# Kernel optimization log

Hardware: AMD Instinct MI355X
Metric: run time of the kernel (lower is better)

Reference implementation:

```python
import jax, jax.numpy as jnp
import numpy as np

B, NQ, NA, C, L = 8, 2048, 64, 128, 4  # batches, queries/mol, atoms/mol, hidden, num_layers
CUTOFF = 8.0
E_AQ, E_QQ = 131072, 262144


def _ln(x, g, b):
    m = x.mean(-1, keepdims=True)
    v = ((x - m) ** 2).mean(-1, keepdims=True)
    return (x - m) * jax.lax.rsqrt(v + 1e-5) * g + b


def _egnn(p, h_src, h_tgt, pos_src, pos_tgt, t_emb, esrc, etgt):
    (mW1, mb1, mW2, mb2, cW1, cb1, cW2, cb2, nW1, nb1, nW2, nb2, g, b) = p
    rel = pos_tgt[etgt] - pos_src[esrc]                      # (E,3)
    sq = (rel ** 2).sum(-1, keepdims=True)                   # (E,1)
    mi = jnp.concatenate([h_src[esrc], h_tgt[etgt], sq, t_emb[etgt]], -1)  # (E,3C+1)
    msg = jax.nn.silu(jax.nn.silu(mi @ mW1 + mb1) @ mW2 + mb2)             # (E,C)
    w = jnp.tanh(jax.nn.silu(msg @ cW1 + cb1) @ cW2 + cb2)                 # (E,1)
    vel = jnp.zeros_like(pos_tgt).at[etgt].add(w * rel)
    agg = jnp.zeros_like(h_tgt).at[etgt].add(msg)
    u = jnp.concatenate([h_tgt, agg], -1)
    h_new = _ln(h_tgt + (jax.nn.silu(u @ nW1 + nb1) @ nW2 + nb2), g, b)
    return h_new, vel


def setup_inputs() -> dict:
    key = jax.random.key(0)
    ks = iter(jax.random.split(key, 64))
    n = lambda shape, s=0.05: jax.random.normal(next(ks), shape, dtype=jnp.float32) * s
    NQT, NAT = B * NQ, B * NA
    return dict(
        x_t=jax.random.normal(next(ks), (NQT, 3), dtype=jnp.float32) * 3.0,
        t_query=jax.random.uniform(next(ks), (NQT,), dtype=jnp.float32),
        atom_pos=jax.random.normal(next(ks), (NAT, 3), dtype=jnp.float32) * 3.0,
        atom_feat=n((NAT, 256), 1.0),
        edge_aq_src=jax.random.randint(next(ks), (E_AQ,), 0, NAT, dtype=jnp.int32),
        edge_aq_tgt=jax.random.randint(next(ks), (E_AQ,), 0, NQT, dtype=jnp.int32),
        edge_qq_src=jax.random.randint(next(ks), (E_QQ,), 0, NQT, dtype=jnp.int32),
        edge_qq_tgt=jax.random.randint(next(ks), (E_QQ,), 0, NQT, dtype=jnp.int32),
        atom_proj_W=n((256, C)), atom_proj_b=jnp.zeros((C,)),
        time_W1=n((C, 4 * C)), time_b1=jnp.zeros((4 * C,)),
        time_W2=n((4 * C, C)), time_b2=jnp.zeros((C,)),
        qi_W1=n((1, C)), qi_b1=jnp.zeros((C,)),
        qi_W2=n((C, C)), qi_b2=jnp.zeros((C,)),
        msg_W1=n((2 * L, 3 * C + 1, 2 * C)), msg_b1=jnp.zeros((2 * L, 2 * C)),
        msg_W2=n((2 * L, 2 * C, C)), msg_b2=jnp.zeros((2 * L, C)),
        cw_W1=n((2 * L, C, C // 2)), cw_b1=jnp.zeros((2 * L, C // 2)),
        cw_W2=n((2 * L, C // 2, 1)), cw_b2=jnp.zeros((2 * L, 1)),
        nu_W1=n((2 * L, 2 * C, C)), nu_b1=jnp.zeros((2 * L, C)),
        nu_W2=n((2 * L, C, C)), nu_b2=jnp.zeros((2 * L, C)),
        ln_g=jnp.ones((2 * L, C)), ln_b=jnp.zeros((2 * L, C)),
        vo_W1=n((C, C)), vo_b1=jnp.zeros((C,)),
        vo_W2=n((C, 1)), vo_b2=jnp.zeros((1,)),
    )


def reference(x_t, t_query, atom_pos, atom_feat,
              edge_aq_src, edge_aq_tgt, edge_qq_src, edge_qq_tgt,
              atom_proj_W, atom_proj_b,
              time_W1, time_b1, time_W2, time_b2,
              qi_W1, qi_b1, qi_W2, qi_b2,
              msg_W1, msg_b1, msg_W2, msg_b2,
              cw_W1, cw_b1, cw_W2, cw_b2,
              nu_W1, nu_b1, nu_W2, nu_b2,
              ln_g, ln_b,
              vo_W1, vo_b1, vo_W2, vo_b2):
    # atom features (no condition drop: eval mode)
    h_atom = atom_feat @ atom_proj_W + atom_proj_b

    # sinusoidal time embedding per query node
    half = C // 2
    freqs = jnp.exp(-np.log(10000.0) * jnp.arange(half, dtype=jnp.float32) / (half - 1))
    args = t_query[:, None] * freqs[None, :]
    emb = jnp.concatenate([jnp.sin(args), jnp.cos(args)], -1)
    t_emb = jax.nn.silu(emb @ time_W1 + time_b1) @ time_W2 + time_b2

    # init query features: log1p(mean_dist / cutoff), equal-size batches
    q = x_t.reshape(B, NQ, 3)
    a = atom_pos.reshape(B, NA, 3)
    sq = ((q[:, :, None, :] - a[:, None, :, :]) ** 2).sum(-1)  # (B,NQ,NA)
    log_dist = jnp.log1p(jnp.sqrt(sq.mean(-1)) / CUTOFF).reshape(-1, 1)
    h = jax.nn.silu(log_dist @ qi_W1 + qi_b1) @ qi_W2 + qi_b2

    layers = (msg_W1, msg_b1, msg_W2, msg_b2, cw_W1, cw_b1, cw_W2, cw_b2,
              nu_W1, nu_b1, nu_W2, nu_b2, ln_g, ln_b)
    pick = lambda j: tuple(arr[j] for arr in layers)

    vel = jnp.zeros_like(x_t)
    for i in range(L):
        h, dv = _egnn(pick(2 * i), h_atom, h, atom_pos, x_t, t_emb, edge_aq_src, edge_aq_tgt)
        vel = vel + dv
        h, dv = _egnn(pick(2 * i + 1), h, h, x_t, x_t, t_emb, edge_qq_src, edge_qq_tgt)
        vel = vel + dv

    scale = jax.nn.silu(h @ vo_W1 + vo_b1) @ vo_W2 + vo_b2   # (N_q,1)
    return vel * scale
```

## Files before the change

kernel.cpp:

```cpp
#include <hip/hip_runtime.h>

#define NQT 16384
#define NAT 512
#define EAQ 131072
#define EQQ 262144

typedef short short8 __attribute__((ext_vector_type(8)));
typedef float float4v __attribute__((ext_vector_type(4)));

__device__ __forceinline__ float silu_f(float x){ return x / (1.f + __expf(-x)); }

__device__ __forceinline__ short f2bf(float f){
  union { float f; unsigned u; } v; v.f = f;
  unsigned r = v.u + 0x7fff + ((v.u >> 16) & 1);
  return (short)(r >> 16);
}
__device__ __forceinline__ float bf2f(short s){
  union { unsigned u; float f; } v;
  v.u = ((unsigned)(unsigned short)s) << 16;
  return v.f;
}

__global__ __launch_bounds__(256) void k_hist(
    const int* __restrict__ etgt, int* __restrict__ hist, int E)
{
  int i = blockIdx.x*256 + threadIdx.x;
  if (i < E) atomicAdd(&hist[etgt[i]], 1);
}

__global__ __launch_bounds__(256) void k_scan(int* __restrict__ hist)
{
  __shared__ int part[256];
  int t = threadIdx.x;
  int base = t * 64;
  int s = 0;
  for (int i = 0; i < 64; i++) s += hist[base + i];
  part[t] = s;
  __syncthreads();
  for (int off = 1; off < 256; off <<= 1){
    int v = (t >= off) ? part[t - off] : 0;
    __syncthreads();
    part[t] += v;
    __syncthreads();
  }
  int run = (t == 0) ? 0 : part[t-1];
  for (int i = 0; i < 64; i++){
    int h = hist[base + i];
    hist[base + i] = run;
    run += h;
  }
}

__global__ __launch_bounds__(256) void k_place(
    const int* __restrict__ esrc, const int* __restrict__ etgt,
    int* __restrict__ cursor, int2* __restrict__ desc, int E)
{
  int i = blockIdx.x*256 + threadIdx.x;
  if (i < E){
    int tg = etgt[i];
    int pos = atomicAdd(&cursor[tg], 1);
    desc[pos] = make_int2(esrc[i], tg);
  }
}

__global__ __launch_bounds__(256) void k_pack(
    const float* __restrict__ W, short* __restrict__ out,
    int rows, int cols, int ksteps, int ntiles, int total, int mode)
{
  int idx = blockIdx.x * 256 + threadIdx.x;
  if (idx >= total) return;
  int l8   = idx & 7;
  int lane = (idx >> 3) & 63;
  int kk   = (idx >> 9) % ksteps;
  int nt   = ((idx >> 9) / ksteps) % ntiles;
  int j    = idx / (512 * ksteps * ntiles);
  int k = kk*32 + (lane >> 4)*8 + l8;
  if (mode == 1) k += (k >= 256);
  else if (mode == 2) k = (k < 128) ? k + 128 : k + 129;
  int n = nt*16 + (lane & 15);
  out[idx] = f2bf(W[(size_t)j*rows*cols + (size_t)k*cols + n]);
}

template<int KSTEPS>
__global__ __launch_bounds__(256) void k_pre(
    const float* __restrict__ Xa, const float* __restrict__ Xb,
    const float* __restrict__ bias,
    const short* __restrict__ Wp, short* __restrict__ out)
{
  int t = threadIdx.x;
  int lane = t & 63, w = t >> 6;
  int mrow = lane & 15, quad = lane >> 4;
  int m0 = blockIdx.x*64 + w*16;

  short8 areg[KSTEPS];
  #pragma unroll
  for (int kk = 0; kk < KSTEPS; kk++){
    int k = kk*32 + quad*8;
    const float* bp;
    if (KSTEPS == 8 && kk >= 4) bp = Xb + (size_t)(m0+mrow)*128 + (k - 128);
    else                        bp = Xa + (size_t)(m0+mrow)*128 + k;
    float4 f0 = *(const float4*)(bp);
    float4 f1 = *(const float4*)(bp + 4);
    short8 s;
    s[0]=f2bf(f0.x); s[1]=f2bf(f0.y); s[2]=f2bf(f0.z); s[3]=f2bf(f0.w);
    s[4]=f2bf(f1.x); s[5]=f2bf(f1.y); s[6]=f2bf(f1.z); s[7]=f2bf(f1.w);
    areg[kk] = s;
  }
  #pragma unroll
  for (int nt = 0; nt < 16; nt++){
    float4v acc = {0.f,0.f,0.f,0.f};
    const short8* Bb = (const short8*)(Wp + ((size_t)nt*KSTEPS)*512 + lane*8);
    #pragma unroll
    for (int kk = 0; kk < KSTEPS; kk++)
      acc = __builtin_amdgcn_mfma_f32_16x16x32_bf16(areg[kk], Bb[kk*64], acc, 0, 0, 0);
    float bv = bias ? bias[nt*16 + mrow] : 0.f;
    #pragma unroll
    for (int r = 0; r < 4; r++)
      out[(size_t)(m0 + quad*4 + r)*256 + nt*16 + mrow] = f2bf(acc[r] + bv);
  }
}

__global__ __launch_bounds__(128) void k_hatom(
    const float* __restrict__ feat, const float* __restrict__ W,
    const float* __restrict__ b, float* __restrict__ out)
{
  __shared__ float sf[256];
  int n = blockIdx.x, t = threadIdx.x;
  sf[t]       = feat[n*256 + t];
  sf[t + 128] = feat[n*256 + 128 + t];
  __syncthreads();
  float acc = b[t];
  for (int k = 0; k < 256; k++) acc += sf[k] * W[k*128 + t];
  out[n*128 + t] = acc;
}

__global__ __launch_bounds__(256) void k_temb(
    const float* __restrict__ tq,
    const short* __restrict__ W1p, const float* __restrict__ b1,
    const short* __restrict__ W2p, const float* __restrict__ b2,
    float* __restrict__ temb)
{
  __shared__ __align__(16) short A[32*136];
  __shared__ __align__(16) short B[32*528];
  int t = threadIdx.x;
  int n0 = blockIdx.x * 32;

  {
    int row = t >> 3, l = t & 7;
    float tv = tq[n0 + row];
    short* o = A + row*136;
    #pragma unroll
    for (int i = 0; i < 16; i++){
      int k = l*16 + i;
      int h = k & 63;
      float freq = __expf(-9.210340371976184f * (float)h * (1.f/63.f));
      float a = tv * freq;
      float v = (k < 64) ? __sinf(a) : __cosf(a);
      o[k] = f2bf(v);
    }
  }
  __syncthreads();

  int lane = t & 63, w = t >> 6;
  int mrow = lane & 15, quad = lane >> 4;

  for (int nti = 0; nti < 8; nti++){
    int nt = w*8 + nti;
    #pragma unroll
    for (int mt = 0; mt < 2; mt++){
      float4v acc = {0.f,0.f,0.f,0.f};
      const short8* Ab = (const short8*)(A + (mt*16 + mrow)*136 + quad*8);
      const short8* Bb = (const short8*)(W1p + (size_t)nt*4*512 + lane*8);
      #pragma unroll
      for (int kk = 0; kk < 4; kk++)
        acc = __builtin_amdgcn_mfma_f32_16x16x32_bf16(Ab[kk*4], Bb[kk*64], acc, 0, 0, 0);
      int n = nt*16 + mrow;
      float b1n = b1[n];
      #pragma unroll
      for (int r = 0; r < 4; r++)
        B[(mt*16 + quad*4 + r)*528 + n] = f2bf(silu_f(acc[r] + b1n));
    }
  }
  __syncthreads();

  #pragma unroll
  for (int nti = 0; nti < 2; nti++){
    int nt = w*2 + nti;
    #pragma unroll
    for (int mt = 0; mt < 2; mt++){
      float4v acc = {0.f,0.f,0.f,0.f};
      const short8* Ab = (const short8*)(B + (mt*16 + mrow)*528 + quad*8);
      const short8* Bb = (const short8*)(W2p + (size_t)nt*16*512 + lane*8);
      #pragma unroll
      for (int kk = 0; kk < 16; kk++)
        acc = __builtin_amdgcn_mfma_f32_16x16x32_bf16(Ab[kk*4], Bb[kk*64], acc, 0, 0, 0);
      int n = nt*16 + mrow;
      float b2n = b2[n];
      #pragma unroll
      for (int r = 0; r < 4; r++)
        temb[(size_t)(n0 + mt*16 + quad*4 + r)*128 + n] = acc[r] + b2n;
    }
  }
}

__global__ __launch_bounds__(128) void k_hinit(
    const float* __restrict__ x_t, const float* __restrict__ atom_pos,
    const float* __restrict__ W1, const float* __restrict__ b1,
    const float* __restrict__ W2, const float* __restrict__ b2,
    float* __restrict__ h)
{
  __shared__ float sh[128];
  __shared__ float sld;
  int n = blockIdx.x, t = threadIdx.x;
  float qx = x_t[n*3], qy = x_t[n*3+1], qz = x_t[n*3+2];
  float part = 0.f;
  if (t < 64){
    int a = (n >> 11)*64 + t;
    float dx = qx - atom_pos[a*3];
    float dy = qy - atom_pos[a*3+1];
    float dz = qz - atom_pos[a*3+2];
    part = dx*dx + dy*dy + dz*dz;
  }
  #pragma unroll
  for (int off = 32; off; off >>= 1) part += __shfl_down(part, off);
  if (t == 0) sld = log1pf(sqrtf(part * (1.f/64.f)) * 0.125f);
  __syncthreads();
  float ld = sld;
  sh[t] = silu_f(ld * W1[t] + b1[t]);
  __syncthreads();
  float acc = b2[t];
  for (int k = 0; k < 128; k++) acc += sh[k] * W2[k*128 + t];
  h[(size_t)n*128 + t] = acc;
}

__global__ __launch_bounds__(256) void k_edge(
    const short* __restrict__ Psrc, const short* __restrict__ Ptgt,
    const float* __restrict__ pos_src, const float* __restrict__ pos_tgt,
    const int2* __restrict__ sdesc,
    const float* __restrict__ w1sq,
    const short* __restrict__ W2p, const float* __restrict__ b2,
    const short* __restrict__ W3p, const float* __restrict__ b3,
    const float* __restrict__ W4,  const float* __restrict__ b4,
    float* __restrict__ agg, float* __restrict__ vel)
{
  __shared__ __align__(16) short A2[32*264];
  __shared__ __align__(16) short A3[32*136];
  __shared__ float sw1[256];
  __shared__ float rel_s[32*3];
  __shared__ int   tgt_s[32];
  float* h3 = (float*)A2;

  int t = threadIdx.x;
  int e0 = blockIdx.x * 32;

  sw1[t] = w1sq[t];
  __syncthreads();

  {
    int e = t >> 3, l = t & 7;
    int2 d = sdesc[e0 + e];
    int src = d.x, tgt = d.y;
    float rx = pos_tgt[tgt*3+0] - pos_src[src*3+0];
    float ry = pos_tgt[tgt*3+1] - pos_src[src*3+1];
    float rz = pos_tgt[tgt*3+2] - pos_src[src*3+2];
    float sqv = rx*rx + ry*ry + rz*rz;
    if (l == 0){
      rel_s[e*3+0]=rx; rel_s[e*3+1]=ry; rel_s[e*3+2]=rz;
      tgt_s[e] = tgt;
    }
    const short8* ps = (const short8*)(Psrc + (size_t)src*256);
    const short8* pt = (const short8*)(Ptgt + (size_t)tgt*256);
    #pragma unroll
    for (int c = 0; c < 4; c++){
      int ci = c*8 + l;
      int n0 = ci*8;
      short8 a = ps[ci], b = pt[ci];
      short8 r;
      #pragma unroll
      for (int j = 0; j < 8; j++){
        int n = n0 + j;
        float v = bf2f(a[j]) + bf2f(b[j]) + sqv*sw1[n];
        r[j] = f2bf(silu_f(v));
      }
      *(short8*)(A2 + e*264 + n0) = r;
    }
  }
  __syncthreads();

  int lane = t & 63, w = t >> 6;
  int mrow = lane & 15, quad = lane >> 4;

  float4v acc2[2][2];
  #pragma unroll
  for (int nti = 0; nti < 2; nti++){
    int nt = w*2 + nti;
    #pragma unroll
    for (int mt = 0; mt < 2; mt++){
      float4v acc = {0.f,0.f,0.f,0.f};
      const short8* Ab = (const short8*)(A2 + (mt*16 + mrow)*264 + quad*8);
      const short8* Bb = (const short8*)(W2p + (size_t)nt*8*512 + lane*8);
      #pragma unroll
      for (int kk = 0; kk < 8; kk++)
        acc = __builtin_amdgcn_mfma_f32_16x16x32_bf16(Ab[kk*4], Bb[kk*64], acc, 0, 0, 0);
      acc2[nti][mt] = acc;
    }
  }

  #pragma unroll
  for (int nti = 0; nti < 2; nti++){
    int nt = w*2 + nti;
    int n = nt*16 + mrow;
    float b2n = b2[n];
    #pragma unroll
    for (int mt = 0; mt < 2; mt++){
      #pragma unroll
      for (int r = 0; r < 4; r++){
        int e = mt*16 + quad*4 + r;
        A3[e*136 + n] = f2bf(silu_f(acc2[nti][mt][r] + b2n));
      }
    }
  }
  __syncthreads();

  {
    int c = t & 127, hh = t >> 7;
    int eb = hh*16;
    float run = 0.f;
    int cur = tgt_s[eb];
    for (int e = eb; e < eb + 16; e++){
      int tg = tgt_s[e];
      if (tg != cur){
        atomicAdd(&agg[(size_t)cur*128 + c], run);
        run = 0.f; cur = tg;
      }
      run += bf2f(A3[e*136 + c]);
    }
    atomicAdd(&agg[(size_t)cur*128 + c], run);
  }
  __syncthreads();

  {
    int nt = w;
    #pragma unroll
    for (int mt = 0; mt < 2; mt++){
      float4v acc = {0.f,0.f,0.f,0.f};
      const short8* Ab = (const short8*)(A3 + (mt*16 + mrow)*136 + quad*8);
      const short8* Bb = (const short8*)(W3p + (size_t)nt*4*512 + lane*8);
      #pragma unroll
      for (int kk = 0; kk < 4; kk++)
        acc = __builtin_amdgcn_mfma_f32_16x16x32_bf16(Ab[kk*4], Bb[kk*64], acc, 0, 0, 0);
      int n = nt*16 + mrow;
      float b3n = b3[n];
      #pragma unroll
      for (int r = 0; r < 4; r++){
        int e = mt*16 + quad*4 + r;
        h3[e*68 + n] = silu_f(acc[r] + b3n);
      }
    }
  }
  __syncthreads();

  {
    int e = t >> 3, l = t & 7;
    float p = 0.f;
    #pragma unroll
    for (int i = 0; i < 8; i++){
      int k = l + 8*i;
      p += h3[e*68 + k] * W4[k];
    }
    p += __shfl_xor(p, 1);
    p += __shfl_xor(p, 2);
    p += __shfl_xor(p, 4);
    if (l == 0){
      float wv = tanhf(p + b4[0]);
      int tg = tgt_s[e];
      atomicAdd(&vel[tg*3+0], wv*rel_s[e*3+0]);
      atomicAdd(&vel[tg*3+1], wv*rel_s[e*3+1]);
      atomicAdd(&vel[tg*3+2], wv*rel_s[e*3+2]);
    }
  }
}

__global__ __launch_bounds__(256) void k_node(
    const float* __restrict__ h, const float* __restrict__ agg,
    const short* __restrict__ W1p, const float* __restrict__ b1,
    const short* __restrict__ W2p, const float* __restrict__ b2,
    const float* __restrict__ g, const float* __restrict__ bb_,
    float* __restrict__ h_out)
{
  __shared__ __align__(16) short A[32*264];
  __shared__ __align__(16) short B[32*136];
  float* r = (float*)A;
  int t = threadIdx.x;
  int n0 = blockIdx.x * 32;

  {
    int row = t >> 3, l = t & 7;
    const float4* hr = (const float4*)(h   + (size_t)(n0+row)*128);
    const float4* ar = (const float4*)(agg + (size_t)(n0+row)*128);
    short* o = A + row*264;
    #pragma unroll
    for (int i = 0; i < 4; i++){
      int k4 = l + 8*i;
      float4 a = hr[k4], b = ar[k4];
      short8 s;
      s[0]=f2bf(a.x); s[1]=f2bf(a.y); s[2]=f2bf(a.z); s[3]=f2bf(a.w);
      s[4]=f2bf(b.x); s[5]=f2bf(b.y); s[6]=f2bf(b.z); s[7]=f2bf(b.w);
      *(short8*)(o + k4*4)       = (short8){s[0],s[1],s[2],s[3],0,0,0,0};
    }
  }
  {
    int row = t >> 3, l = t & 7;
    const float4* hr = (const float4*)(h   + (size_t)(n0+row)*128);
    const float4* ar = (const float4*)(agg + (size_t)(n0+row)*128);
    short* o = A + row*264;
    #pragma unroll
    for (int i = 0; i < 4; i++){
      int k4 = l + 8*i;
      float4 a = hr[k4];
      short4 s4;
      short sa0=f2bf(a.x), sa1=f2bf(a.y), sa2=f2bf(a.z), sa3=f2bf(a.w);
      o[k4*4+0]=sa0; o[k4*4+1]=sa1; o[k4*4+2]=sa2; o[k4*4+3]=sa3;
      float4 b = ar[k4];
      o[128 + k4*4+0]=f2bf(b.x); o[128 + k4*4+1]=f2bf(b.y);
      o[128 + k4*4+2]=f2bf(b.z); o[128 + k4*4+3]=f2bf(b.w);
    }
  }
  __syncthreads();

  int lane = t & 63, w = t >> 6;
  int mrow = lane & 15, quad = lane >> 4;

  float4v accA[2][2];
  #pragma unroll
  for (int nti = 0; nti < 2; nti++){
    int nt = w*2 + nti;
    #pragma unroll
    for (int mt = 0; mt < 2; mt++){
      float4v acc = {0.f,0.f,0.f,0.f};
      const short8* Ab = (const short8*)(A + (mt*16 + mrow)*264 + quad*8);
      const short8* Bb = (const short8*)(W1p + (size_t)nt*8*512 + lane*8);
      #pragma unroll
      for (int kk = 0; kk < 8; kk++)
        acc = __builtin_amdgcn_mfma_f32_16x16x32_bf16(Ab[kk*4], Bb[kk*64], acc, 0, 0, 0);
      accA[nti][mt] = acc;
    }
  }
  __syncthreads();

  #pragma unroll
  for (int nti = 0; nti < 2; nti++){
    int n = (w*2 + nti)*16 + mrow;
    float b1n = b1[n];
    #pragma unroll
    for (int mt = 0; mt < 2; mt++){
      #pragma unroll
      for (int rr = 0; rr < 4; rr++){
        int e = mt*16 + quad*4 + rr;
        B[e*136 + n] = f2bf(silu_f(accA[nti][mt][rr] + b1n));
      }
    }
  }
  __syncthreads();

  #pragma unroll
  for (int nti = 0; nti < 2; nti++){
    int nt = w*2 + nti;
    #pragma unroll
    for (int mt = 0; mt < 2; mt++){
      float4v acc = {0.f,0.f,0.f,0.f};
      const short8* Ab = (const short8*)(B + (mt*16 + mrow)*136 + quad*8);
      const short8* Bb = (const short8*)(W2p + (size_t)nt*4*512 + lane*8);
      #pragma unroll
      for (int kk = 0; kk < 4; kk++)
        acc = __builtin_amdgcn_mfma_f32_16x16x32_bf16(Ab[kk*4], Bb[kk*64], acc, 0, 0, 0);
      int n = nt*16 + mrow;
      float b2n = b2[n];
      #pragma unroll
      for (int rr = 0; rr < 4; rr++){
        int e = mt*16 + quad*4 + rr;
        r[e*132 + n] = h[(size_t)(n0+e)*128 + n] + acc[rr] + b2n;
      }
    }
  }
  __syncthreads();

  {
    int lane2 = t & 63, wid = t >> 6;
    #pragma unroll
    for (int nn = 0; nn < 8; nn++){
      int row = wid*8 + nn;
      float a = r[row*132 + lane2], bv = r[row*132 + lane2 + 64];
      float s = a + bv, ss = a*a + bv*bv;
      #pragma unroll
      for (int off = 1; off < 64; off <<= 1){
        s  += __shfl_xor(s, off);
        ss += __shfl_xor(ss, off);
      }
      float mean = s * (1.f/128.f);
      float var  = ss * (1.f/128.f) - mean*mean;
      float rstd = rsqrtf(var + 1e-5f);
      float* ho = h_out + (size_t)(n0+row)*128;
      ho[lane2]      = (a  - mean)*rstd*g[lane2]      + bb_[lane2];
      ho[lane2 + 64] = (bv - mean)*rstd*g[lane2 + 64] + bb_[lane2 + 64];
    }
  }
}

__global__ __launch_bounds__(128) void k_out(
    const float* __restrict__ h, const float* __restrict__ vel,
    const float* __restrict__ W1, const float* __restrict__ b1,
    const float* __restrict__ W2, const float* __restrict__ b2,
    float* __restrict__ out)
{
  __shared__ float sh[128];
  __shared__ float spart[2];
  int n = blockIdx.x, t = threadIdx.x;
  sh[t] = h[(size_t)n*128 + t];
  __syncthreads();
  float acc = b1[t];
  for (int k = 0; k < 128; k++) acc += sh[k] * W1[k*128 + t];
  float p = silu_f(acc) * W2[t];
  #pragma unroll
  for (int off = 32; off; off >>= 1) p += __shfl_down(p, off);
  if ((t & 63) == 0) spart[t >> 6] = p;
  __syncthreads();
  if (t < 3){
    float scale = spart[0] + spart[1] + b2[0];
    out[n*3 + t] = vel[n*3 + t] * scale;
  }
}

extern "C" void kernel_launch(void* const* d_in, const int* in_sizes, int n_in,
                              void* d_out, int out_size, void* d_ws, size_t ws_size,
                              hipStream_t stream)
{
  const float* x_t       = (const float*)d_in[0];
  const float* t_query   = (const float*)d_in[1];
  const float* atom_pos  = (const float*)d_in[2];
  const float* atom_feat = (const float*)d_in[3];
  const int*   e_aq_s = (const int*)d_in[4];
  const int*   e_aq_t = (const int*)d_in[5];
  const int*   e_qq_s = (const int*)d_in[6];
  const int*   e_qq_t = (const int*)d_in[7];
  const float* apW  = (const float*)d_in[8];
  const float* apb  = (const float*)d_in[9];
  const float* tW1  = (const float*)d_in[10];
  const float* tb1  = (const float*)d_in[11];
  const float* tW2  = (const float*)d_in[12];
  const float* tb2  = (const float*)d_in[13];
  const float* qiW1 = (const float*)d_in[14];
  const float* qib1 = (const float*)d_in[15];
  const float* qiW2 = (const float*)d_in[16];
  const float* qib2 = (const float*)d_in[17];
  const float* mW1  = (const float*)d_in[18];
  const float* mb1  = (const float*)d_in[19];
  const float* mW2  = (const float*)d_in[20];
  const float* mb2  = (const float*)d_in[21];
  const float* cW1  = (const float*)d_in[22];
  const float* cb1  = (const float*)d_in[23];
  const float* cW2  = (const float*)d_in[24];
  const float* cb2  = (const float*)d_in[25];
  const float* nW1  = (const float*)d_in[26];
  const float* nb1  = (const float*)d_in[27];
  const float* nW2  = (const float*)d_in[28];
  const float* nb2  = (const float*)d_in[29];
  const float* lng  = (const float*)d_in[30];
  const float* lnb  = (const float*)d_in[31];
  const float* voW1 = (const float*)d_in[32];
  const float* vob1 = (const float*)d_in[33];
  const float* voW2 = (const float*)d_in[34];
  const float* vob2 = (const float*)d_in[35];
  float* out = (float*)d_out;

  float* ws     = (float*)d_ws;
  float* h_atom = ws;
  float* temb   = h_atom + 65536;
  float* hA     = temb + 2097152;
  float* hB     = hA + 2097152;
  float* agg    = hB + 2097152;
  float* vel    = agg + 2097152;
  short* W1ap   = (short*)(vel + 49152);
  short* W1bcp  = W1ap + 262144;
  short* W2p    = W1bcp + 524288;
  short* W3p    = W2p + 262144;
  short* nW1p   = W3p + 65536;
  short* nW2p   = nW1p + 262144;
  short* tW1p   = nW2p + 131072;
  short* tW2p   = tW1p + 65536;
  short* Psrc   = tW2p + 65536;
  short* Ptgt   = Psrc + 4194304;
  int*   hist_a = (int*)(Ptgt + 4194304);
  int*   hist_q = hist_a + 16384;
  int2*  desc_a = (int2*)(hist_q + 16384);
  int2*  desc_q = desc_a + EAQ;

  hipMemsetAsync(hist_a, 0, 16384*sizeof(int), stream);
  hipMemsetAsync(hist_q, 0, 16384*sizeof(int), stream);
  k_hist<<<EAQ/256, 256, 0, stream>>>(e_aq_t, hist_a, EAQ);
  k_hist<<<EQQ/256, 256, 0, stream>>>(e_qq_t, hist_q, EQQ);
  k_scan<<<1, 256, 0, stream>>>(hist_a);
  k_scan<<<1, 256, 0, stream>>>(hist_q);
  k_place<<<EAQ/256, 256, 0, stream>>>(e_aq_s, e_aq_t, hist_a, desc_a, EAQ);
  k_place<<<EQQ/256, 256, 0, stream>>>(e_qq_s, e_qq_t, hist_q, desc_q, EQQ);

  k_pack<<<(262144+255)/256, 256, 0, stream>>>(mW1, W1ap,  385, 256, 4, 16, 262144, 0);
  k_pack<<<(524288+255)/256, 256, 0, stream>>>(mW1, W1bcp, 385, 256, 8, 16, 524288, 2);
  k_pack<<<(262144+255)/256, 256, 0, stream>>>(mW2, W2p,   256, 128, 8,  8, 262144, 0);
  k_pack<<<( 65536+255)/256, 256, 0, stream>>>(cW1, W3p,   128,  64, 4,  4,  65536, 0);
  k_pack<<<(262144+255)/256, 256, 0, stream>>>(nW1, nW1p,  256, 128, 8,  8, 262144, 0);
  k_pack<<<(131072+255)/256, 256, 0, stream>>>(nW2, nW2p,  128, 128, 4,  8, 131072, 0);
  k_pack<<<( 65536+255)/256, 256, 0, stream>>>(tW1, tW1p,  128, 512, 4, 32,  65536, 0);
  k_pack<<<( 65536+255)/256, 256, 0, stream>>>(tW2, tW2p,  512, 128, 16, 8,  65536, 0);

  hipMemsetAsync(vel, 0, (size_t)NQT*3*sizeof(float), stream);
  k_hatom<<<NAT, 128, 0, stream>>>(atom_feat, apW, apb, h_atom);
  k_temb<<<NQT/32, 256, 0, stream>>>(t_query, tW1p, tb1, tW2p, tb2, temb);
  k_hinit<<<NQT, 128, 0, stream>>>(x_t, atom_pos, qiW1, qib1, qiW2, qib2, hA);

  float* hc = hA; float* hn = hB;
  for (int i = 0; i < 4; i++){
    for (int half = 0; half < 2; half++){
      int j = 2*i + half;
      const int2* dsc = half ? desc_q : desc_a;
      int E = half ? EQQ : EAQ;
      const float* hsrc = half ? hc : h_atom;
      int Msrc = half ? NQT : NAT;

      k_pre<4><<<Msrc/64, 256, 0, stream>>>(hsrc, nullptr, nullptr,
          W1ap + (size_t)j*32768, Psrc);
      k_pre<8><<<NQT/64, 256, 0, stream>>>(hc, temb, mb1 + (size_t)j*256,
          W1bcp + (size_t)j*65536, Ptgt);

      hipMemsetAsync(agg, 0, (size_t)NQT*128*sizeof(float), stream);
      k_edge<<<E/32, 256, 0, stream>>>(Psrc, Ptgt,
          half ? x_t : atom_pos, x_t, dsc,
          mW1 + (size_t)j*385*256 + 65536,
          W2p + (size_t)j*32768, mb2 + (size_t)j*128,
          W3p + (size_t)j*8192,  cb1 + (size_t)j*64,
          cW2 + (size_t)j*64,    cb2 + (size_t)j,
          agg, vel);
      k_node<<<NQT/32, 256, 0, stream>>>(hc, agg,
          nW1p + (size_t)j*32768, nb1 + (size_t)j*128,
          nW2p + (size_t)j*16384, nb2 + (size_t)j*128,
          lng + (size_t)j*128,    lnb + (size_t)j*128, hn);
      float* tmp = hc; hc = hn; hn = tmp;
    }
  }
  k_out<<<NQT, 128, 0, stream>>>(hc, vel, voW1, vob1, voW2, vob2, out);
}
```

Before: 1.433 ms.

## Merge setup launches, fuse pre-GEMMs, widen edge kernel, zero agg in node kernel

Merges the histogram, scan, place and weight-pack launches into single kernels, and fuses the two per-layer projection GEMMs into one launch to cut launch overhead. The edge kernel moves to 512 threads with one n-tile per wave and reads the squared-distance weight directly from global memory instead of staging it in shared memory. Messages are aggregated from an fp32 copy rather than bf16, and the coordinate-MLP MFMA is issued before the scatter. The node kernel now zeroes agg after reading it, which removes the per-layer memset, so correctness depends on the first memset also covering agg and vel.

```diff
diff --git a/kernel.cpp b/kernel.cpp
--- a/kernel.cpp
+++ b/kernel.cpp
@@ -21,15 +21,18 @@
   return v.f;
 }
 
-__global__ __launch_bounds__(256) void k_hist(
-    const int* __restrict__ etgt, int* __restrict__ hist, int E)
+__global__ __launch_bounds__(256) void k_hist2(
+    const int* __restrict__ ta, const int* __restrict__ tq,
+    int* __restrict__ ha, int* __restrict__ hq)
 {
   int i = blockIdx.x*256 + threadIdx.x;
-  if (i < E) atomicAdd(&hist[etgt[i]], 1);
-}
-
-__global__ __launch_bounds__(256) void k_scan(int* __restrict__ hist)
-{
+  atomicAdd(&hq[tq[i]], 1);
+  if (i < EAQ) atomicAdd(&ha[ta[i]], 1);
+}
+
+__global__ __launch_bounds__(256) void k_scan2(int* __restrict__ ha, int* __restrict__ hq)
+{
+  int* hist = (blockIdx.x == 0) ? ha : hq;
   __shared__ int part[256];
   int t = threadIdx.x;
   int base = t * 64;
@@ -51,24 +54,21 @@
   }
 }
 
-__global__ __launch_bounds__(256) void k_place(
-    const int* __restrict__ esrc, const int* __restrict__ etgt,
-    int* __restrict__ cursor, int2* __restrict__ desc, int E)
+__global__ __launch_bounds__(256) void k_place2(
+    const int* __restrict__ sa, const int* __restrict__ ta,
+    const int* __restrict__ sq, const int* __restrict__ tq,
+    int* __restrict__ ca, int* __restrict__ cq,
+    int2* __restrict__ da, int2* __restrict__ dq)
 {
   int i = blockIdx.x*256 + threadIdx.x;
-  if (i < E){
-    int tg = etgt[i];
-    int pos = atomicAdd(&cursor[tg], 1);
-    desc[pos] = make_int2(esrc[i], tg);
-  }
-}
-
-__global__ __launch_bounds__(256) void k_pack(
+  { int tg = tq[i]; int pos = atomicAdd(&cq[tg], 1); dq[pos] = make_int2(sq[i], tg); }
+  if (i < EAQ){ int tg = ta[i]; int pos = atomicAdd(&ca[tg], 1); da[pos] = make_int2(sa[i], tg); }
+}
+
+__device__ __forceinline__ void pack_one(
     const float* __restrict__ W, short* __restrict__ out,
-    int rows, int cols, int ksteps, int ntiles, int total, int mode)
-{
-  int idx = blockIdx.x * 256 + threadIdx.x;
-  if (idx >= total) return;
+    int rows, int cols, int ksteps, int ntiles, int idx, int mode)
+{
   int l8   = idx & 7;
   int lane = (idx >> 3) & 63;
   int kk   = (idx >> 9) % ksteps;
@@ -81,42 +81,86 @@
   out[idx] = f2bf(W[(size_t)j*rows*cols + (size_t)k*cols + n]);
 }
 
-template<int KSTEPS>
-__global__ __launch_bounds__(256) void k_pre(
-    const float* __restrict__ Xa, const float* __restrict__ Xb,
-    const float* __restrict__ bias,
-    const short* __restrict__ Wp, short* __restrict__ out)
+__global__ __launch_bounds__(256) void k_packall(
+    const float* __restrict__ mW1, const float* __restrict__ mW2,
+    const float* __restrict__ cW1, const float* __restrict__ nW1,
+    const float* __restrict__ nW2, const float* __restrict__ tW1,
+    const float* __restrict__ tW2,
+    short* W1ap, short* W1bcp, short* W2p, short* W3p,
+    short* nW1p, short* nW2p, short* tW1p, short* tW2p)
+{
+  int b = blockIdx.x, t = threadIdx.x;
+  if (b < 1024){ pack_one(mW1, W1ap, 385,256,4,16, b*256+t, 0); return; } b -= 1024;
+  if (b < 2048){ pack_one(mW1, W1bcp,385,256,8,16, b*256+t, 2); return; } b -= 2048;
+  if (b < 1024){ pack_one(mW2, W2p,  256,128,8, 8, b*256+t, 0); return; } b -= 1024;
+  if (b <  256){ pack_one(cW1, W3p,  128, 64,4, 4, b*256+t, 0); return; } b -=  256;
+  if (b < 1024){ pack_one(nW1, nW1p, 256,128,8, 8, b*256+t, 0); return; } b -= 1024;
+  if (b <  512){ pack_one(nW2, nW2p, 128,128,4, 8, b*256+t, 0); return; } b -=  512;
+  if (b <  256){ pack_one(tW1, tW1p, 128,512,4,32, b*256+t, 0); return; } b -=  256;
+  pack_one(tW2, tW2p, 512,128,16,8, b*256+t, 0);
+}
+
+__global__ __launch_bounds__(256) void k_pre2(
+    const float* __restrict__ Xsrc, const float* __restrict__ Xh,
+    const float* __restrict__ Xt, const float* __restrict__ biasT,
+    const short* __restrict__ WpA, const short* __restrict__ WpB,
+    short* __restrict__ Psrc, short* __restrict__ Ptgt, int nblkA)
 {
   int t = threadIdx.x;
   int lane = t & 63, w = t >> 6;
   int mrow = lane & 15, quad = lane >> 4;
-  int m0 = blockIdx.x*64 + w*16;
-
-  short8 areg[KSTEPS];
-  #pragma unroll
-  for (int kk = 0; kk < KSTEPS; kk++){
-    int k = kk*32 + quad*8;
-    const float* bp;
-    if (KSTEPS == 8 && kk >= 4) bp = Xb + (size_t)(m0+mrow)*128 + (k - 128);
-    else                        bp = Xa + (size_t)(m0+mrow)*128 + k;
-    float4 f0 = *(const float4*)(bp);
-    float4 f1 = *(const float4*)(bp + 4);
-    short8 s;
-    s[0]=f2bf(f0.x); s[1]=f2bf(f0.y); s[2]=f2bf(f0.z); s[3]=f2bf(f0.w);
-    s[4]=f2bf(f1.x); s[5]=f2bf(f1.y); s[6]=f2bf(f1.z); s[7]=f2bf(f1.w);
-    areg[kk] = s;
-  }
-  #pragma unroll
-  for (int nt = 0; nt < 16; nt++){
-    float4v acc = {0.f,0.f,0.f,0.f};
-    const short8* Bb = (const short8*)(Wp + ((size_t)nt*KSTEPS)*512 + lane*8);
-    #pragma unroll
-    for (int kk = 0; kk < KSTEPS; kk++)
-      acc = __builtin_amdgcn_mfma_f32_16x16x32_bf16(areg[kk], Bb[kk*64], acc, 0, 0, 0);
-    float bv = bias ? bias[nt*16 + mrow] : 0.f;
-    #pragma unroll
-    for (int r = 0; r < 4; r++)
-      out[(size_t)(m0 + quad*4 + r)*256 + nt*16 + mrow] = f2bf(acc[r] + bv);
+
+  if ((int)blockIdx.x < nblkA){
+    int m0 = blockIdx.x*64 + w*16;
+    short8 areg[4];
+    #pragma unroll
+    for (int kk = 0; kk < 4; kk++){
+      const float* bp = Xsrc + (size_t)(m0+mrow)*128 + kk*32 + quad*8;
+      float4 f0 = *(const float4*)(bp);
+      float4 f1 = *(const float4*)(bp + 4);
+      short8 s;
+      s[0]=f2bf(f0.x); s[1]=f2bf(f0.y); s[2]=f2bf(f0.z); s[3]=f2bf(f0.w);
+      s[4]=f2bf(f1.x); s[5]=f2bf(f1.y); s[6]=f2bf(f1.z); s[7]=f2bf(f1.w);
+      areg[kk] = s;
+    }
+    #pragma unroll
+    for (int nt = 0; nt < 16; nt++){
+      float4v acc = {0.f,0.f,0.f,0.f};
+      const short8* Bb = (const short8*)(WpA + ((size_t)nt*4)*512 + lane*8);
+      #pragma unroll
+      for (int kk = 0; kk < 4; kk++)
+        acc = __builtin_amdgcn_mfma_f32_16x16x32_bf16(areg[kk], Bb[kk*64], acc, 0, 0, 0);
+      #pragma unroll
+      for (int r = 0; r < 4; r++)
+        Psrc[(size_t)(m0 + quad*4 + r)*256 + nt*16 + mrow] = f2bf(acc[r]);
+    }
+  } else {
+    int m0 = ((int)blockIdx.x - nblkA)*64 + w*16;
+    short8 areg[8];
+    #pragma unroll
+    for (int kk = 0; kk < 8; kk++){
+      int k = kk*32 + quad*8;
+      const float* bp = (kk >= 4) ? (Xt + (size_t)(m0+mrow)*128 + (k - 128))
+                                  : (Xh + (size_t)(m0+mrow)*128 + k);
+      float4 f0 = *(const float4*)(bp);
+      float4 f1 = *(const float4*)(bp + 4);
+      short8 s;
+      s[0]=f2bf(f0.x); s[1]=f2bf(f0.y); s[2]=f2bf(f0.z); s[3]=f2bf(f0.w);
+      s[4]=f2bf(f1.x); s[5]=f2bf(f1.y); s[6]=f2bf(f1.z); s[7]=f2bf(f1.w);
+      areg[kk] = s;
+    }
+    #pragma unroll
+    for (int nt = 0; nt < 16; nt++){
+      float4v acc = {0.f,0.f,0.f,0.f};
+      const short8* Bb = (const short8*)(WpB + ((size_t)nt*8)*512 + lane*8);
+      #pragma unroll
+      for (int kk = 0; kk < 8; kk++)
+        acc = __builtin_amdgcn_mfma_f32_16x16x32_bf16(areg[kk], Bb[kk*64], acc, 0, 0, 0);
+      float bv = biasT[nt*16 + mrow];
+      #pragma unroll
+      for (int r = 0; r < 4; r++)
+        Ptgt[(size_t)(m0 + quad*4 + r)*256 + nt*16 + mrow] = f2bf(acc[r] + bv);
+    }
   }
 }
 
@@ -233,7 +277,7 @@
   h[(size_t)n*128 + t] = acc;
 }
 
-__global__ __launch_bounds__(256) void k_edge(
+__global__ __launch_bounds__(512, 8) void k_edge(
     const short* __restrict__ Psrc, const short* __restrict__ Ptgt,
     const float* __restrict__ pos_src, const float* __restrict__ pos_tgt,
     const int2* __restrict__ sdesc,
@@ -245,19 +289,16 @@
 {
   __shared__ __align__(16) short A2[32*264];
   __shared__ __align__(16) short A3[32*136];
-  __shared__ float sw1[256];
   __shared__ float rel_s[32*3];
   __shared__ int   tgt_s[32];
-  float* h3 = (float*)A2;
+  float* msgf = (float*)A2;
+  float* h3   = (float*)A2;
 
   int t = threadIdx.x;
   int e0 = blockIdx.x * 32;
 
-  sw1[t] = w1sq[t];
-  __syncthreads();
-
-  {
-    int e = t >> 3, l = t & 7;
+  {
+    int e = t >> 4, l = t & 15;
     int2 d = sdesc[e0 + e];
     int src = d.x, tgt = d.y;
     float rx = pos_tgt[tgt*3+0] - pos_src[src*3+0];
@@ -271,17 +312,21 @@
     const short8* ps = (const short8*)(Psrc + (size_t)src*256);
     const short8* pt = (const short8*)(Ptgt + (size_t)tgt*256);
     #pragma unroll
-    for (int c = 0; c < 4; c++){
-      int ci = c*8 + l;
+    for (int c = 0; c < 2; c++){
+      int ci = l + 16*c;
       int n0 = ci*8;
       short8 a = ps[ci], b = pt[ci];
+      float4 w0 = *(const float4*)(w1sq + n0);
+      float4 w1 = *(const float4*)(w1sq + n0 + 4);
       short8 r;
-      #pragma unroll
-      for (int j = 0; j < 8; j++){
-        int n = n0 + j;
-        float v = bf2f(a[j]) + bf2f(b[j]) + sqv*sw1[n];
-        r[j] = f2bf(silu_f(v));
-      }
+      r[0] = f2bf(silu_f(bf2f(a[0]) + bf2f(b[0]) + sqv*w0.x));
+      r[1] = f2bf(silu_f(bf2f(a[1]) + bf2f(b[1]) + sqv*w0.y));
+      r[2] = f2bf(silu_f(bf2f(a[2]) + bf2f(b[2]) + sqv*w0.z));
+      r[3] = f2bf(silu_f(bf2f(a[3]) + bf2f(b[3]) + sqv*w0.w));
+      r[4] = f2bf(silu_f(bf2f(a[4]) + bf2f(b[4]) + sqv*w1.x));
+      r[5] = f2bf(silu_f(bf2f(a[5]) + bf2f(b[5]) + sqv*w1.y));
+      r[6] = f2bf(silu_f(bf2f(a[6]) + bf2f(b[6]) + sqv*w1.z));
+      r[7] = f2bf(silu_f(bf2f(a[7]) + bf2f(b[7]) + sqv*w1.w));
       *(short8*)(A2 + e*264 + n0) = r;
     }
   }
@@ -290,10 +335,9 @@
   int lane = t & 63, w = t >> 6;
   int mrow = lane & 15, quad = lane >> 4;
 
-  float4v acc2[2][2];
-  #pragma unroll
-  for (int nti = 0; nti < 2; nti++){
-    int nt = w*2 + nti;
+  float4v acc2[2];
+  {
+    int nt = w;
     #pragma unroll
     for (int mt = 0; mt < 2; mt++){
       float4v acc = {0.f,0.f,0.f,0.f};
@@ -302,75 +346,78 @@
       #pragma unroll
       for (int kk = 0; kk < 8; kk++)
         acc = __builtin_amdgcn_mfma_f32_16x16x32_bf16(Ab[kk*4], Bb[kk*64], acc, 0, 0, 0);
-      acc2[nti][mt] = acc;
-    }
-  }
-
-  #pragma unroll
-  for (int nti = 0; nti < 2; nti++){
-    int nt = w*2 + nti;
-    int n = nt*16 + mrow;
+      acc2[mt] = acc;
+    }
+  }
+  __syncthreads();
+
+  {
+    int n = w*16 + mrow;
     float b2n = b2[n];
     #pragma unroll
     for (int mt = 0; mt < 2; mt++){
       #pragma unroll
       for (int r = 0; r < 4; r++){
         int e = mt*16 + quad*4 + r;
-        A3[e*136 + n] = f2bf(silu_f(acc2[nti][mt][r] + b2n));
+        float v = silu_f(acc2[mt][r] + b2n);
+        msgf[e*132 + n] = v;
+        A3[e*136 + n]   = f2bf(v);
       }
     }
   }
   __syncthreads();
 
-  {
-    int c = t & 127, hh = t >> 7;
-    int eb = hh*16;
+  int nt3 = w & 3, mt3 = w >> 2;
+  float4v acc3 = {0.f,0.f,0.f,0.f};
+  {
+    const short8* Ab = (const short8*)(A3 + (mt3*16 + mrow)*136 + quad*8);
+    const short8* Bb = (const short8*)(W3p + (size_t)nt3*4*512 + lane*8);
+    #pragma unroll
+    for (int kk = 0; kk < 4; kk++)
+      acc3 = __builtin_amdgcn_mfma_f32_16x16x32_bf16(Ab[kk*4], Bb[kk*64], acc3, 0, 0, 0);
+  }
+
+  {
+    int c = t & 127, g = t >> 7;
+    int eb = g*8;
     float run = 0.f;
     int cur = tgt_s[eb];
-    for (int e = eb; e < eb + 16; e++){
+    #pragma unroll
+    for (int e = eb; e < eb + 8; e++){
       int tg = tgt_s[e];
       if (tg != cur){
         atomicAdd(&agg[(size_t)cur*128 + c], run);
         run = 0.f; cur = tg;
       }
-      run += bf2f(A3[e*136 + c]);
+      run += msgf[e*132 + c];
     }
     atomicAdd(&agg[(size_t)cur*128 + c], run);
   }
   __syncthreads();
 
   {
-    int nt = w;
-    #pragma unroll
-    for (int mt = 0; mt < 2; mt++){
-      float4v acc = {0.f,0.f,0.f,0.f};
-      const short8* Ab = (const short8*)(A3 + (mt*16 + mrow)*136 + quad*8);
-      const short8* Bb = (const short8*)(W3p + (size_t)nt*4*512 + lane*8);
-      #pragma unroll
-      for (int kk = 0; kk < 4; kk++)
-        acc = __builtin_amdgcn_mfma_f32_16x16x32_bf16(Ab[kk*4], Bb[kk*64], acc, 0, 0, 0);
-      int n = nt*16 + mrow;
-      float b3n = b3[n];
-      #pragma unroll
-      for (int r = 0; r < 4; r++){
-        int e = mt*16 + quad*4 + r;
-        h3[e*68 + n] = silu_f(acc[r] + b3n);
-      }
-    }
-  }
-  __syncthreads();
-
-  {
-    int e = t >> 3, l = t & 7;
+    int n = nt3*16 + mrow;
+    float b3n = b3[n];
+    #pragma unroll
+    for (int r = 0; r < 4; r++){
+      int e = mt3*16 + quad*4 + r;
+      h3[e*68 + n] = silu_f(acc3[r] + b3n);
+    }
+  }
+  __syncthreads();
+
+  {
+    int e = t >> 4, l = t & 15;
     float p = 0.f;
     #pragma unroll
-    for (int i = 0; i < 8; i++){
-      int k = l + 8*i;
+    for (int i = 0; i < 4; i++){
+      int k = l + 16*i;
       p += h3[e*68 + k] * W4[k];
     }
     p += __shfl_xor(p, 1);
     p += __shfl_xor(p, 2);
     p += __shfl_xor(p, 4);
+    p += __shfl_xor(p, 8);
     if (l == 0){
       float wv = tanhf(p + b4[0]);
       int tg = tgt_s[e];
@@ -382,7 +429,7 @@
 }
 
 __global__ __launch_bounds__(256) void k_node(
-    const float* __restrict__ h, const float* __restrict__ agg,
+    const float* __restrict__ h, float* __restrict__ agg,
     const short* __restrict__ W1p, const float* __restrict__ b1,
     const short* __restrict__ W2p, const float* __restrict__ b2,
     const float* __restrict__ g, const float* __restrict__ bb_,
@@ -396,34 +443,19 @@
 
   {
     int row = t >> 3, l = t & 7;
-    const float4* hr = (const float4*)(h   + (size_t)(n0+row)*128);
-    const float4* ar = (const float4*)(agg + (size_t)(n0+row)*128);
+    const float4* hr = (const float4*)(h + (size_t)(n0+row)*128);
+    float4*       ar = (float4*)(agg + (size_t)(n0+row)*128);
     short* o = A + row*264;
-    #pragma unroll
-    for (int i = 0; i < 4; i++){
-      int k4 = l + 8*i;
-      float4 a = hr[k4], b = ar[k4];
-      short8 s;
-      s[0]=f2bf(a.x); s[1]=f2bf(a.y); s[2]=f2bf(a.z); s[3]=f2bf(a.w);
-      s[4]=f2bf(b.x); s[5]=f2bf(b.y); s[6]=f2bf(b.z); s[7]=f2bf(b.w);
-      *(short8*)(o + k4*4)       = (short8){s[0],s[1],s[2],s[3],0,0,0,0};
-    }
-  }
-  {
-    int row = t >> 3, l = t & 7;
-    const float4* hr = (const float4*)(h   + (size_t)(n0+row)*128);
-    const float4* ar = (const float4*)(agg + (size_t)(n0+row)*128);
-    short* o = A + row*264;
+    float4 z = make_float4(0.f,0.f,0.f,0.f);
     #pragma unroll
     for (int i = 0; i < 4; i++){
       int k4 = l + 8*i;
       float4 a = hr[k4];
-      short4 s4;
-      short sa0=f2bf(a.x), sa1=f2bf(a.y), sa2=f2bf(a.z), sa3=f2bf(a.w);
-      o[k4*4+0]=sa0; o[k4*4+1]=sa1; o[k4*4+2]=sa2; o[k4*4+3]=sa3;
+      o[k4*4+0]=f2bf(a.x); o[k4*4+1]=f2bf(a.y); o[k4*4+2]=f2bf(a.z); o[k4*4+3]=f2bf(a.w);
       float4 b = ar[k4];
       o[128 + k4*4+0]=f2bf(b.x); o[128 + k4*4+1]=f2bf(b.y);
       o[128 + k4*4+2]=f2bf(b.z); o[128 + k4*4+3]=f2bf(b.w);
+      ar[k4] = z;
     }
   }
   __syncthreads();
@@ -595,25 +627,16 @@
   int2*  desc_a = (int2*)(hist_q + 16384);
   int2*  desc_q = desc_a + EAQ;
 
-  hipMemsetAsync(hist_a, 0, 16384*sizeof(int), stream);
-  hipMemsetAsync(hist_q, 0, 16384*sizeof(int), stream);
-  k_hist<<<EAQ/256, 256, 0, stream>>>(e_aq_t, hist_a, EAQ);
-  k_hist<<<EQQ/256, 256, 0, stream>>>(e_qq_t, hist_q, EQQ);
-  k_scan<<<1, 256, 0, stream>>>(hist_a);
-  k_scan<<<1, 256, 0, stream>>>(hist_q);
-  k_place<<<EAQ/256, 256, 0, stream>>>(e_aq_s, e_aq_t, hist_a, desc_a, EAQ);
-  k_place<<<EQQ/256, 256, 0, stream>>>(e_qq_s, e_qq_t, hist_q, desc_q, EQQ);
-
-  k_pack<<<(262144+255)/256, 256, 0, stream>>>(mW1, W1ap,  385, 256, 4, 16, 262144, 0);
-  k_pack<<<(524288+255)/256, 256, 0, stream>>>(mW1, W1bcp, 385, 256, 8, 16, 524288, 2);
-  k_pack<<<(262144+255)/256, 256, 0, stream>>>(mW2, W2p,   256, 128, 8,  8, 262144, 0);
-  k_pack<<<( 65536+255)/256, 256, 0, stream>>>(cW1, W3p,   128,  64, 4,  4,  65536, 0);
-  k_pack<<<(262144+255)/256, 256, 0, stream>>>(nW1, nW1p,  256, 128, 8,  8, 262144, 0);
-  k_pack<<<(131072+255)/256, 256, 0, stream>>>(nW2, nW2p,  128, 128, 4,  8, 131072, 0);
-  k_pack<<<( 65536+255)/256, 256, 0, stream>>>(tW1, tW1p,  128, 512, 4, 32,  65536, 0);
-  k_pack<<<( 65536+255)/256, 256, 0, stream>>>(tW2, tW2p,  512, 128, 16, 8,  65536, 0);
-
-  hipMemsetAsync(vel, 0, (size_t)NQT*3*sizeof(float), stream);
+  hipMemsetAsync(hist_a, 0, 2*16384*sizeof(int), stream);
+  k_hist2<<<EQQ/256, 256, 0, stream>>>(e_aq_t, e_qq_t, hist_a, hist_q);
+  k_scan2<<<2, 256, 0, stream>>>(hist_a, hist_q);
+  k_place2<<<EQQ/256, 256, 0, stream>>>(e_aq_s, e_aq_t, e_qq_s, e_qq_t,
+                                        hist_a, hist_q, desc_a, desc_q);
+
+  k_packall<<<6400, 256, 0, stream>>>(mW1, mW2, cW1, nW1, nW2, tW1, tW2,
+      W1ap, W1bcp, W2p, W3p, nW1p, nW2p, tW1p, tW2p);
+
+  hipMemsetAsync(agg, 0, (size_t)(NQT*128 + NQT*3)*sizeof(float), stream);
   k_hatom<<<NAT, 128, 0, stream>>>(atom_feat, apW, apb, h_atom);
   k_temb<<<NQT/32, 256, 0, stream>>>(t_query, tW1p, tb1, tW2p, tb2, temb);
   k_hinit<<<NQT, 128, 0, stream>>>(x_t, atom_pos, qiW1, qib1, qiW2, qib2, hA);
@@ -625,15 +648,14 @@
       const int2* dsc = half ? desc_q : desc_a;
       int E = half ? EQQ : EAQ;
       const float* hsrc = half ? hc : h_atom;
-      int Msrc = half ? NQT : NAT;
-
-      k_pre<4><<<Msrc/64, 256, 0, stream>>>(hsrc, nullptr, nullptr,
-          W1ap + (size_t)j*32768, Psrc);
-      k_pre<8><<<NQT/64, 256, 0, stream>>>(hc, temb, mb1 + (size_t)j*256,
-          W1bcp + (size_t)j*65536, Ptgt);
-
-      hipMemsetAsync(agg, 0, (size_t)NQT*128*sizeof(float), stream);
-      k_edge<<<E/32, 256, 0, stream>>>(Psrc, Ptgt,
+      int nblkA = (half ? NQT : NAT) / 64;
+
+      k_pre2<<<nblkA + NQT/64, 256, 0, stream>>>(hsrc, hc, temb,
+          mb1 + (size_t)j*256,
+          W1ap + (size_t)j*32768, W1bcp + (size_t)j*65536,
+          Psrc, Ptgt, nblkA);
+
+      k_edge<<<E/32, 512, 0, stream>>>(Psrc, Ptgt,
           half ? x_t : atom_pos, x_t, dsc,
           mW1 + (size_t)j*385*256 + 65536,
           W2p + (size_t)j*32768, mb2 + (size_t)j*128,
```

After: 1.541 ms. 1.08x slower.
